# Kernel optimization log

Measured on AMD Instinct MI355X. Metric: run time of the kernel, lower is better.

The kernel has to match this reference:

```python
import jax, jax.numpy as jnp
import numpy as np

ALPHA = 0.2  # LeakyReLU negative slope


def setup_inputs() -> dict:
    key = jax.random.key(0)
    k1, k2 = jax.random.split(key)
    B, W, K = 32, 128, 1024
    x = jax.random.normal(k1, (B, W, K), dtype=jnp.float32)
    # xavier_uniform with gain=1.414 on shape (2W, 1)
    fan_in, fan_out = 2 * W, 1
    bound = 1.414 * np.sqrt(6.0 / (fan_in + fan_out))
    w = jax.random.uniform(k2, (2 * W, 1), dtype=jnp.float32, minval=-bound, maxval=bound)
    return {"x": x, "w": w}


def reference(x, w):
    # x: (B, W, K) -> v: (B, K, W)
    v = jnp.transpose(x, (0, 2, 1))
    Wdim = v.shape[-1]
    # concat(v_i, v_j) @ w  ==  v_i @ w[:W] + v_j @ w[W:]
    w1 = w[:Wdim, 0]  # (W,)
    w2 = w[Wdim:, 0]  # (W,)
    s1 = v @ w1  # (B, K)
    s2 = v @ w2  # (B, K)
    e = jax.nn.leaky_relu(s1[:, :, None] + s2[:, None, :], negative_slope=ALPHA)  # (B, K, K)
    attention = jax.nn.softmax(e, axis=2)
    # dropout=0.0 / eval mode -> identity
    h = jnp.einsum('bij,bjw->biw', attention, v)  # (B, K, W)
    return h
```

## Files before the change

kernel.cpp:

```cpp
#include <hip/hip_runtime.h>

#define ALPHA 0.2f

constexpr int WDIM = 128;
constexpr int KDIM = 1024;
constexpr int NSEG = 64;
constexpr int SEGLEN = KDIM / NSEG;

typedef _Float16 h4 __attribute__((ext_vector_type(4)));
typedef _Float16 h8 __attribute__((ext_vector_type(8)));

constexpr int OFF_XTH  = 0;
constexpr int OFF_TABH = 32768;
constexpr int OFF_ESC  = 163968;
constexpr int OFF_ESCA = 164992;
constexpr int OFF_ABT  = 166016;
constexpr int OFF_U    = 168192;
constexpr int OFF_T    = 169216;
constexpr int OFF_S1   = 170240;
constexpr int OFF_S2   = 171264;
constexpr int OFF_CC   = 172288;
constexpr int OFF_PERM = 173312;
constexpr int OFF_TA   = 174336;
constexpr int OFF_TB   = 182528;
constexpr int OFF_SBA  = 190720;
constexpr int OFF_SBB  = 198912;
constexpr int PBF      = 207104;

__global__ __launch_bounds__(256) void k_s12(const float* __restrict__ x,
                                             const float* __restrict__ w,
                                             float* __restrict__ ws, int b0) {
  const int slot = blockIdx.y;
  const int b = b0 + slot;
  float* base = ws + (size_t)slot * PBF;
  __shared__ float w1s[WDIM], w2s[WDIM];
  __shared__ float red1[4][64], red2[4][64];
  int t = threadIdx.x;
  if (t < WDIM) { w1s[t] = w[t]; w2s[t] = w[WDIM + t]; }
  __syncthreads();
  int jj = t & 63, wg = t >> 6;
  int j = blockIdx.x * 64 + jj;
  int w0 = wg * 32;
  const float* xb = x + (size_t)b * (WDIM * KDIM);
  float s1 = 0.f, s2 = 0.f;
  float vals[32];
#pragma unroll
  for (int k = 0; k < 32; ++k) {
    float v = xb[(w0 + k) * KDIM + j];
    vals[k] = v;
    s1 = fmaf(v, w1s[w0 + k], s1);
    s2 = fmaf(v, w2s[w0 + k], s2);
  }
  _Float16* xrowh = (_Float16*)(base + OFF_XTH) + j * WDIM + w0;
#pragma unroll
  for (int q = 0; q < 4; ++q) {
    h8 hv;
#pragma unroll
    for (int e = 0; e < 8; ++e) hv[e] = (_Float16)vals[8 * q + e];
    *(h8*)(xrowh + 8 * q) = hv;
  }
  red1[wg][jj] = s1;
  red2[wg][jj] = s2;
  __syncthreads();
  if (wg == 0) {
    base[OFF_S1 + j] = red1[0][jj] + red1[1][jj] + red1[2][jj] + red1[3][jj];
    base[OFF_S2 + j] = red2[0][jj] + red2[1][jj] + red2[2][jj] + red2[3][jj];
  }
}

__global__ __launch_bounds__(512) void k_rank(float* __restrict__ ws) {
  const int slot = blockIdx.y;
  float* base = ws + (size_t)slot * PBF;
  __shared__ float s2s[KDIM];
  __shared__ float red[512];
  __shared__ int pr[128][4], pc[128][4];
  int t = threadIdx.x;
  for (int i = t; i < KDIM; i += 512) s2s[i] = base[OFF_S2 + i];
  __syncthreads();
  red[t] = fmaxf(s2s[t], s2s[t + 512]);
  __syncthreads();
  for (int s = 256; s > 0; s >>= 1) {
    if (t < s) red[t] = fmaxf(red[t], red[t + s]);
    __syncthreads();
  }
  float M2 = red[0];
  int jj = t >> 2, quarter = t & 3;
  int j = blockIdx.x * 128 + jj;
  float s2me = s2s[j];
  float s1me = base[OFF_S1 + j];
  float key = -s1me;
  int r = 0, c = 0;
  int lo = quarter * 256;
#pragma unroll 4
  for (int k2 = 0; k2 < 256; ++k2) {
    float v = s2s[lo + k2];
    int jp = lo + k2;
    r += (v > s2me || (v == s2me && jp < j)) ? 1 : 0;
    c += (v >= key) ? 1 : 0;
  }
  pr[jj][quarter] = r;
  pc[jj][quarter] = c;
  __syncthreads();
  if (quarter == 0) {
    int R = pr[jj][0] + pr[jj][1] + pr[jj][2] + pr[jj][3];
    int C = pc[jj][0] + pc[jj][1] + pc[jj][2] + pc[jj][3];
    ((int*)(base + OFF_CC))[j] = C;
    ((int*)(base + OFF_PERM))[R] = j;
    base[OFF_ESC + R] = __expf(s2me - M2);
    base[OFF_ESCA + R] = __expf(ALPHA * s2me);
    float z = s1me + M2;
    float mi = z >= 0.f ? z : ALPHA * z;
    base[OFF_U + j] = __expf(z - mi);
    base[OFF_T + j] = __expf(ALPHA * s1me - mi);
  }
}

__global__ __launch_bounds__(256) void k_tot(float* __restrict__ ws) {
  const int slot = blockIdx.y;
  float* base = ws + (size_t)slot * PBF;
  __shared__ float sc[256];
  int t = threadIdx.x;
  int bx = blockIdx.x;
  if (bx < 32) {
    int w = t & 127, sl = t >> 7;
    int seg = bx * 2 + sl;
    int r0 = seg * SEGLEN;
    const _Float16* xTh = (const _Float16*)(base + OFF_XTH);
    const int* prm = (const int*)(base + OFF_PERM);
    int pr16[SEGLEN];
#pragma unroll
    for (int k = 0; k < SEGLEN; ++k) pr16[k] = prm[r0 + k];
    float xv[SEGLEN], eav[SEGLEN], ebv[SEGLEN];
#pragma unroll
    for (int k = 0; k < SEGLEN; ++k) {
      xv[k] = (float)xTh[pr16[k] * WDIM + w];
      eav[k] = base[OFF_ESC + r0 + k];
      ebv[k] = base[OFF_ESCA + r0 + k];
    }
    float ta = 0.f, tb = 0.f;
#pragma unroll
    for (int k = 0; k < SEGLEN; ++k) {
      ta = fmaf(eav[k], xv[k], ta);
      tb = fmaf(ebv[k], xv[k], tb);
    }
    base[OFF_TA + seg * WDIM + w] = ta;
    base[OFF_TB + seg * WDIM + w] = tb;
  } else if (bx == 32) {
    float4 v = *(const float4*)(base + OFF_ESC + 4 * t);
    float p1 = v.x, p2 = p1 + v.y, p3 = p2 + v.z, p4 = p3 + v.w;
    sc[t] = p4;
    __syncthreads();
    for (int s = 1; s < 256; s <<= 1) {
      float add = (t >= s) ? sc[t - s] : 0.f;
      __syncthreads();
      sc[t] += add;
      __syncthreads();
    }
    float bs = (t > 0) ? sc[t - 1] : 0.f;
    float* ABT = base + OFF_ABT;
    ABT[2 * (4 * t + 1)] = bs + p1;
    ABT[2 * (4 * t + 2)] = bs + p2;
    ABT[2 * (4 * t + 3)] = bs + p3;
    ABT[2 * (4 * t + 4)] = bs + p4;
    if (t == 0) ABT[0] = 0.f;
  } else {
    float4 v = *(const float4*)(base + OFF_ESCA + 4 * t);
    float q3 = v.w, q2 = v.z + q3, q1 = v.y + q2, q0 = v.x + q1;
    sc[t] = q0;
    __syncthreads();
    for (int s = 1; s < 256; s <<= 1) {
      float add = (t + s < 256) ? sc[t + s] : 0.f;
      __syncthreads();
      sc[t] += add;
      __syncthreads();
    }
    float bs = (t < 255) ? sc[t + 1] : 0.f;
    float* ABT = base + OFF_ABT;
    ABT[2 * (4 * t + 0) + 1] = bs + q0;
    ABT[2 * (4 * t + 1) + 1] = bs + q1;
    ABT[2 * (4 * t + 2) + 1] = bs + q2;
    ABT[2 * (4 * t + 3) + 1] = bs + q3;
    if (t == 255) ABT[2 * KDIM + 1] = 0.f;
  }
}

__global__ __launch_bounds__(256) void k_base(float* __restrict__ ws) {
  float* base = ws + (size_t)blockIdx.x * PBF;
  __shared__ float gA[2][128], gB[2][128];
  int t = threadIdx.x;
  int w = t & 127, h = t >> 7;
  float ta32[32], tb32[32];
  float ga = 0.f, gb = 0.f;
#pragma unroll
  for (int k = 0; k < 32; ++k) {
    ta32[k] = base[OFF_TA + (h * 32 + k) * WDIM + w];
    tb32[k] = base[OFF_TB + (h * 32 + k) * WDIM + w];
    ga += ta32[k];
    gb += tb32[k];
  }
  gA[h][w] = ga;
  gB[h][w] = gb;
  __syncthreads();
  float bA = (h == 1) ? gA[0][w] : 0.f;
  float bB = (h == 0) ? gB[1][w] : 0.f;
#pragma unroll
  for (int k = 0; k < 32; ++k) {
    base[OFF_SBA + (h * 32 + k) * WDIM + w] = bA;
    bA += ta32[k];
  }
#pragma unroll
  for (int k = 31; k >= 0; --k) {
    base[OFF_SBB + (h * 32 + k) * WDIM + w] = bB;
    bB += tb32[k];
  }
}

__global__ __launch_bounds__(128) void k_scan(float* __restrict__ ws) {
  const int slot = blockIdx.y;
  float* base = ws + (size_t)slot * PBF;
  int seg = blockIdx.x;
  int wl = threadIdx.x;
  int r0 = seg * SEGLEN;
  const _Float16* xTh = (const _Float16*)(base + OFF_XTH);
  const int* prm = (const int*)(base + OFF_PERM);
  int pr16[SEGLEN];
#pragma unroll
  for (int k = 0; k < SEGLEN; ++k) pr16[k] = prm[r0 + k];
  float xv[SEGLEN], eav[SEGLEN], ebv[SEGLEN];
#pragma unroll
  for (int k = 0; k < SEGLEN; ++k) {
    xv[k] = (float)xTh[pr16[k] * WDIM + wl];
    eav[k] = base[OFF_ESC + r0 + k];
    ebv[k] = base[OFF_ESCA + r0 + k];
  }
  _Float16* TABh = (_Float16*)(base + OFF_TABH);
  float accA = base[OFF_SBA + seg * WDIM + wl];
#pragma unroll
  for (int k = 0; k < SEGLEN; ++k) {
    TABh[(r0 + k) * 256 + wl] = (_Float16)accA;
    accA = fmaf(eav[k], xv[k], accA);
  }
  if (seg == NSEG - 1) TABh[KDIM * 256 + wl] = (_Float16)accA;
  float accB = base[OFF_SBB + seg * WDIM + wl];
#pragma unroll
  for (int k = SEGLEN - 1; k >= 0; --k) {
    accB = fmaf(ebv[k], xv[k], accB);
    TABh[(r0 + k) * 256 + 128 + wl] = (_Float16)accB;
  }
  if (seg == 0) TABh[KDIM * 256 + 128 + wl] = (_Float16)0.f;
}

__global__ __launch_bounds__(256) void k_out(const float* __restrict__ ws,
                                             float* __restrict__ out, int b0) {
  const int slot = blockIdx.y;
  const int b = b0 + slot;
  const float* base = ws + (size_t)slot * PBF;
  int q = blockIdx.x * 256 + threadIdx.x;
  int i = q >> 5;
  int wq = (q & 31) << 2;
  int c = ((const int*)(base + OFF_CC))[i];
  float u = base[OFF_U + i];
  float tt = base[OFF_T + i];
  float2 ab = *(const float2*)(base + OFF_ABT + 2 * c);
  float rden = 1.f / fmaf(u, ab.x, tt * ab.y);
  const _Float16* TABh = (const _Float16*)(base + OFF_TABH);
  h4 A4 = *(const h4*)(TABh + (size_t)c * 256 + wq);
  h4 B4 = *(const h4*)(TABh + (size_t)c * 256 + 128 + wq);
  float4 o;
  o.x = (u * (float)A4[0] + tt * (float)B4[0]) * rden;
  o.y = (u * (float)A4[1] + tt * (float)B4[1]) * rden;
  o.z = (u * (float)A4[2] + tt * (float)B4[2]) * rden;
  o.w = (u * (float)A4[3] + tt * (float)B4[3]) * rden;
  *(float4*)(out + (size_t)b * (KDIM * WDIM) + (size_t)q * 4) = o;
}

extern "C" void kernel_launch(void* const* d_in, const int* in_sizes, int n_in,
                              void* d_out, int out_size, void* d_ws, size_t ws_size,
                              hipStream_t stream) {
  const float* x = (const float*)d_in[0];
  const float* w = (const float*)d_in[1];
  float* out = (float*)d_out;
  float* ws = (float*)d_ws;
  const int NB = 32;
  size_t perb = (size_t)PBF * sizeof(float);
  int nbmax = (int)(ws_size / perb);
  if (nbmax < 1) nbmax = 1;
  if (nbmax > NB) nbmax = NB;
  for (int b0 = 0; b0 < NB; b0 += nbmax) {
    int nb = (NB - b0 < nbmax) ? (NB - b0) : nbmax;
    k_s12<<<dim3(16, nb), 256, 0, stream>>>(x, w, ws, b0);
    k_rank<<<dim3(8, nb), 512, 0, stream>>>(ws);
    k_tot<<<dim3(34, nb), 256, 0, stream>>>(ws);
    k_base<<<nb, 256, 0, stream>>>(ws);
    k_scan<<<dim3(NSEG, nb), 128, 0, stream>>>(ws);
    k_out<<<dim3(128, nb), 256, 0, stream>>>(ws, out, b0);
  }
}
```

Measured before the change: 47.83 us.

## Fuse prefix-table scan into output kernel, drop the global fp16 table

Drops the global fp16 prefix table (TABh). Each output block now rebuilds its segment's prefix sums in shared memory and writes outputs for the rows whose rank falls in that segment. A new rank-sorted row list and per-segment row ranges are computed in k_mid/k_base so k_fout can find its rows. This removes one kernel launch and the global write/read round trip of the table, and shrinks the workspace so more batches fit per pass. The cost is uneven work per block, since segments hold different row counts, plus serial per-row loops with only 128 threads per block.

```diff
diff --git a/kernel.cpp b/kernel.cpp
--- a/kernel.cpp
+++ b/kernel.cpp
@@ -7,25 +7,25 @@
 constexpr int NSEG = 64;
 constexpr int SEGLEN = KDIM / NSEG;
 
-typedef _Float16 h4 __attribute__((ext_vector_type(4)));
 typedef _Float16 h8 __attribute__((ext_vector_type(8)));
 
 constexpr int OFF_XTH  = 0;
-constexpr int OFF_TABH = 32768;
-constexpr int OFF_ESC  = 163968;
-constexpr int OFF_ESCA = 164992;
-constexpr int OFF_ABT  = 166016;
-constexpr int OFF_U    = 168192;
-constexpr int OFF_T    = 169216;
-constexpr int OFF_S1   = 170240;
-constexpr int OFF_S2   = 171264;
-constexpr int OFF_CC   = 172288;
-constexpr int OFF_PERM = 173312;
-constexpr int OFF_TA   = 174336;
-constexpr int OFF_TB   = 182528;
-constexpr int OFF_SBA  = 190720;
-constexpr int OFF_SBB  = 198912;
-constexpr int PBF      = 207104;
+constexpr int OFF_ESC  = 65536;
+constexpr int OFF_ESCA = 66560;
+constexpr int OFF_ABT  = 67584;
+constexpr int OFF_U    = 69760;
+constexpr int OFF_T    = 70784;
+constexpr int OFF_S1   = 71808;
+constexpr int OFF_S2   = 72832;
+constexpr int OFF_CC   = 73856;
+constexpr int OFF_PERM = 74880;
+constexpr int OFF_LIST = 75904;
+constexpr int OFF_SEGS = 76928;
+constexpr int OFF_TA   = 77056;
+constexpr int OFF_TB   = 85248;
+constexpr int OFF_SBA  = 93440;
+constexpr int OFF_SBB  = 101632;
+constexpr int PBF      = 109824;
 
 __global__ __launch_bounds__(256) void k_s12(const float* __restrict__ x,
                                              const float* __restrict__ w,
@@ -115,15 +115,16 @@
   }
 }
 
-__global__ __launch_bounds__(256) void k_tot(float* __restrict__ ws) {
+__global__ __launch_bounds__(512) void k_mid(float* __restrict__ ws) {
   const int slot = blockIdx.y;
   float* base = ws + (size_t)slot * PBF;
-  __shared__ float sc[256];
+  __shared__ int ccs[KDIM];
+  __shared__ int pr[128][4];
   int t = threadIdx.x;
   int bx = blockIdx.x;
-  if (bx < 32) {
-    int w = t & 127, sl = t >> 7;
-    int seg = bx * 2 + sl;
+  if (bx < 16) {
+    int slice = t >> 7, wl = t & 127;
+    int seg = bx * 4 + slice;
     int r0 = seg * SEGLEN;
     const _Float16* xTh = (const _Float16*)(base + OFF_XTH);
     const int* prm = (const int*)(base + OFF_PERM);
@@ -133,7 +134,7 @@
     float xv[SEGLEN], eav[SEGLEN], ebv[SEGLEN];
 #pragma unroll
     for (int k = 0; k < SEGLEN; ++k) {
-      xv[k] = (float)xTh[pr16[k] * WDIM + w];
+      xv[k] = (float)xTh[pr16[k] * WDIM + wl];
       eav[k] = base[OFF_ESC + r0 + k];
       ebv[k] = base[OFF_ESCA + r0 + k];
     }
@@ -143,9 +144,64 @@
       ta = fmaf(eav[k], xv[k], ta);
       tb = fmaf(ebv[k], xv[k], tb);
     }
-    base[OFF_TA + seg * WDIM + w] = ta;
-    base[OFF_TB + seg * WDIM + w] = tb;
-  } else if (bx == 32) {
+    base[OFF_TA + seg * WDIM + wl] = ta;
+    base[OFF_TB + seg * WDIM + wl] = tb;
+  } else {
+    const int* CC = (const int*)(base + OFF_CC);
+    for (int i = t; i < KDIM; i += 512) ccs[i] = CC[i];
+    __syncthreads();
+    int jj = t >> 2, quarter = t & 3;
+    int i = (bx - 16) * 128 + jj;
+    int ci = ccs[i];
+    int r = 0;
+    int lo = quarter * 256;
+#pragma unroll 4
+    for (int k2 = 0; k2 < 256; ++k2) {
+      int cv = ccs[lo + k2];
+      int ip = lo + k2;
+      r += (cv < ci || (cv == ci && ip < i)) ? 1 : 0;
+    }
+    pr[jj][quarter] = r;
+    __syncthreads();
+    if (quarter == 0) {
+      int R = pr[jj][0] + pr[jj][1] + pr[jj][2] + pr[jj][3];
+      ((int*)(base + OFF_LIST))[R] = i;
+    }
+  }
+}
+
+__global__ __launch_bounds__(256) void k_base(float* __restrict__ ws) {
+  float* base = ws + (size_t)blockIdx.y * PBF;
+  __shared__ float gA[2][128], gB[2][128];
+  __shared__ float sc[256];
+  int t = threadIdx.x;
+  if (blockIdx.x == 0) {
+    int w = t & 127, h = t >> 7;
+    float ta32[32], tb32[32];
+    float ga = 0.f, gb = 0.f;
+#pragma unroll
+    for (int k = 0; k < 32; ++k) {
+      ta32[k] = base[OFF_TA + (h * 32 + k) * WDIM + w];
+      tb32[k] = base[OFF_TB + (h * 32 + k) * WDIM + w];
+      ga += ta32[k];
+      gb += tb32[k];
+    }
+    gA[h][w] = ga;
+    gB[h][w] = gb;
+    __syncthreads();
+    float bA = (h == 1) ? gA[0][w] : 0.f;
+    float bB = (h == 0) ? gB[1][w] : 0.f;
+#pragma unroll
+    for (int k = 0; k < 32; ++k) {
+      base[OFF_SBA + (h * 32 + k) * WDIM + w] = bA;
+      bA += ta32[k];
+    }
+#pragma unroll
+    for (int k = 31; k >= 0; --k) {
+      base[OFF_SBB + (h * 32 + k) * WDIM + w] = bB;
+      bB += tb32[k];
+    }
+  } else if (blockIdx.x == 1) {
     float4 v = *(const float4*)(base + OFF_ESC + 4 * t);
     float p1 = v.x, p2 = p1 + v.y, p3 = p2 + v.z, p4 = p3 + v.w;
     sc[t] = p4;
@@ -163,7 +219,7 @@
     ABT[2 * (4 * t + 3)] = bs + p3;
     ABT[2 * (4 * t + 4)] = bs + p4;
     if (t == 0) ABT[0] = 0.f;
-  } else {
+  } else if (blockIdx.x == 2) {
     float4 v = *(const float4*)(base + OFF_ESCA + 4 * t);
     float q3 = v.w, q2 = v.z + q3, q1 = v.y + q2, q0 = v.x + q1;
     sc[t] = q0;
@@ -181,97 +237,96 @@
     ABT[2 * (4 * t + 2) + 1] = bs + q2;
     ABT[2 * (4 * t + 3) + 1] = bs + q3;
     if (t == 255) ABT[2 * KDIM + 1] = 0.f;
-  }
-}
-
-__global__ __launch_bounds__(256) void k_base(float* __restrict__ ws) {
-  float* base = ws + (size_t)blockIdx.x * PBF;
-  __shared__ float gA[2][128], gB[2][128];
-  int t = threadIdx.x;
-  int w = t & 127, h = t >> 7;
-  float ta32[32], tb32[32];
-  float ga = 0.f, gb = 0.f;
-#pragma unroll
-  for (int k = 0; k < 32; ++k) {
-    ta32[k] = base[OFF_TA + (h * 32 + k) * WDIM + w];
-    tb32[k] = base[OFF_TB + (h * 32 + k) * WDIM + w];
-    ga += ta32[k];
-    gb += tb32[k];
-  }
-  gA[h][w] = ga;
-  gB[h][w] = gb;
-  __syncthreads();
-  float bA = (h == 1) ? gA[0][w] : 0.f;
-  float bB = (h == 0) ? gB[1][w] : 0.f;
-#pragma unroll
-  for (int k = 0; k < 32; ++k) {
-    base[OFF_SBA + (h * 32 + k) * WDIM + w] = bA;
-    bA += ta32[k];
-  }
-#pragma unroll
-  for (int k = 31; k >= 0; --k) {
-    base[OFF_SBB + (h * 32 + k) * WDIM + w] = bB;
-    bB += tb32[k];
-  }
-}
-
-__global__ __launch_bounds__(128) void k_scan(float* __restrict__ ws) {
-  const int slot = blockIdx.y;
-  float* base = ws + (size_t)slot * PBF;
-  int seg = blockIdx.x;
-  int wl = threadIdx.x;
-  int r0 = seg * SEGLEN;
-  const _Float16* xTh = (const _Float16*)(base + OFF_XTH);
-  const int* prm = (const int*)(base + OFF_PERM);
-  int pr16[SEGLEN];
-#pragma unroll
-  for (int k = 0; k < SEGLEN; ++k) pr16[k] = prm[r0 + k];
-  float xv[SEGLEN], eav[SEGLEN], ebv[SEGLEN];
-#pragma unroll
-  for (int k = 0; k < SEGLEN; ++k) {
-    xv[k] = (float)xTh[pr16[k] * WDIM + wl];
-    eav[k] = base[OFF_ESC + r0 + k];
-    ebv[k] = base[OFF_ESCA + r0 + k];
-  }
-  _Float16* TABh = (_Float16*)(base + OFF_TABH);
-  float accA = base[OFF_SBA + seg * WDIM + wl];
-#pragma unroll
-  for (int k = 0; k < SEGLEN; ++k) {
-    TABh[(r0 + k) * 256 + wl] = (_Float16)accA;
-    accA = fmaf(eav[k], xv[k], accA);
-  }
-  if (seg == NSEG - 1) TABh[KDIM * 256 + wl] = (_Float16)accA;
-  float accB = base[OFF_SBB + seg * WDIM + wl];
-#pragma unroll
-  for (int k = SEGLEN - 1; k >= 0; --k) {
-    accB = fmaf(ebv[k], xv[k], accB);
-    TABh[(r0 + k) * 256 + 128 + wl] = (_Float16)accB;
-  }
-  if (seg == 0) TABh[KDIM * 256 + 128 + wl] = (_Float16)0.f;
-}
-
-__global__ __launch_bounds__(256) void k_out(const float* __restrict__ ws,
-                                             float* __restrict__ out, int b0) {
+  } else {
+    const int* LIST = (const int*)(base + OFF_LIST);
+    const int* CC = (const int*)(base + OFF_CC);
+    int* SEGS = (int*)(base + OFF_SEGS);
+#pragma unroll
+    for (int e = 0; e < 4; ++e) {
+      int rr = 4 * t + e;
+      int cL = CC[LIST[rr]] >> 4; if (cL > NSEG - 1) cL = NSEG - 1;
+      int cP = -1;
+      if (rr > 0) { cP = CC[LIST[rr - 1]] >> 4; if (cP > NSEG - 1) cP = NSEG - 1; }
+      for (int bb = cP + 1; bb <= cL; ++bb) SEGS[bb] = rr;
+      if (rr == KDIM - 1)
+        for (int bb = cL + 1; bb <= NSEG; ++bb) SEGS[bb] = KDIM;
+    }
+  }
+}
+
+__global__ __launch_bounds__(128) void k_fout(const float* __restrict__ ws,
+                                              float* __restrict__ out, int b0) {
   const int slot = blockIdx.y;
   const int b = b0 + slot;
   const float* base = ws + (size_t)slot * PBF;
-  int q = blockIdx.x * 256 + threadIdx.x;
-  int i = q >> 5;
-  int wq = (q & 31) << 2;
-  int c = ((const int*)(base + OFF_CC))[i];
-  float u = base[OFF_U + i];
-  float tt = base[OFF_T + i];
-  float2 ab = *(const float2*)(base + OFF_ABT + 2 * c);
-  float rden = 1.f / fmaf(u, ab.x, tt * ab.y);
-  const _Float16* TABh = (const _Float16*)(base + OFF_TABH);
-  h4 A4 = *(const h4*)(TABh + (size_t)c * 256 + wq);
-  h4 B4 = *(const h4*)(TABh + (size_t)c * 256 + 128 + wq);
-  float4 o;
-  o.x = (u * (float)A4[0] + tt * (float)B4[0]) * rden;
-  o.y = (u * (float)A4[1] + tt * (float)B4[1]) * rden;
-  o.z = (u * (float)A4[2] + tt * (float)B4[2]) * rden;
-  o.w = (u * (float)A4[3] + tt * (float)B4[3]) * rden;
-  *(float4*)(out + (size_t)b * (KDIM * WDIM) + (size_t)q * 4) = o;
+  int s = blockIdx.x;
+  int wl = threadIdx.x;
+  int r0 = s * SEGLEN;
+  __shared__ float pA[SEGLEN + 1][WDIM], pB[SEGLEN + 1][WDIM];
+  __shared__ int sh_i[128], sh_m[128];
+  __shared__ float sh_u[128], sh_t[128];
+  __shared__ float2 sh_ab[128];
+
+  const _Float16* xTh = (const _Float16*)(base + OFF_XTH);
+  const int* prm = (const int*)(base + OFF_PERM);
+  const int* LIST = (const int*)(base + OFF_LIST);
+  const int* CC = (const int*)(base + OFF_CC);
+
+  int pr16[SEGLEN];
+#pragma unroll
+  for (int k = 0; k < SEGLEN; ++k) pr16[k] = prm[r0 + k];
+  float eav[SEGLEN], ebv[SEGLEN], xv[SEGLEN];
+#pragma unroll
+  for (int k = 0; k < SEGLEN; ++k) {
+    eav[k] = base[OFF_ESC + r0 + k];
+    ebv[k] = base[OFF_ESCA + r0 + k];
+  }
+#pragma unroll
+  for (int k = 0; k < SEGLEN; ++k) xv[k] = (float)xTh[pr16[k] * WDIM + wl];
+
+  float accA = base[OFF_SBA + s * WDIM + wl];
+#pragma unroll
+  for (int k = 0; k < SEGLEN; ++k) {
+    pA[k][wl] = accA;
+    accA = fmaf(eav[k], xv[k], accA);
+  }
+  pA[SEGLEN][wl] = accA;
+  float accB = base[OFF_SBB + s * WDIM + wl];
+  pB[SEGLEN][wl] = accB;
+#pragma unroll
+  for (int k = SEGLEN - 1; k >= 0; --k) {
+    accB = fmaf(ebv[k], xv[k], accB);
+    pB[k][wl] = accB;
+  }
+  __syncthreads();
+
+  const int* SEGS = (const int*)(base + OFF_SEGS);
+  int rs = SEGS[s], re = SEGS[s + 1];
+
+  float* ob = out + (size_t)b * (KDIM * WDIM);
+  const float* ABT = base + OFF_ABT;
+  for (int rc = rs; rc < re; rc += 128) {
+    int nr = min(128, re - rc);
+    if (wl < nr) {
+      int r = rc + wl;
+      int i = LIST[r];
+      int c = CC[i];
+      sh_i[wl] = i;
+      sh_m[wl] = c - r0;
+      sh_u[wl] = base[OFF_U + i];
+      sh_t[wl] = base[OFF_T + i];
+      sh_ab[wl] = *(const float2*)&ABT[2 * c];
+    }
+    __syncthreads();
+    for (int q = 0; q < nr; ++q) {
+      float u = sh_u[q], tt = sh_t[q];
+      float2 ab = sh_ab[q];
+      float rden = 1.f / fmaf(u, ab.x, tt * ab.y);
+      int m = sh_m[q];
+      ob[(size_t)sh_i[q] * WDIM + wl] = (u * pA[m][wl] + tt * pB[m][wl]) * rden;
+    }
+    __syncthreads();
+  }
 }
 
 extern "C" void kernel_launch(void* const* d_in, const int* in_sizes, int n_in,
@@ -290,9 +345,8 @@
     int nb = (NB - b0 < nbmax) ? (NB - b0) : nbmax;
     k_s12<<<dim3(16, nb), 256, 0, stream>>>(x, w, ws, b0);
     k_rank<<<dim3(8, nb), 512, 0, stream>>>(ws);
-    k_tot<<<dim3(34, nb), 256, 0, stream>>>(ws);
-    k_base<<<nb, 256, 0, stream>>>(ws);
-    k_scan<<<dim3(NSEG, nb), 128, 0, stream>>>(ws);
-    k_out<<<dim3(128, nb), 256, 0, stream>>>(ws, out, b0);
-  }
-}
+    k_mid<<<dim3(24, nb), 512, 0, stream>>>(ws);
+    k_base<<<dim3(4, nb), 256, 0, stream>>>(ws);
+    k_fout<<<dim3(NSEG, nb), 128, 0, stream>>>(ws, out, b0);
+  }
+}
```

Result: slower. 54.41 us (+13.8%).
